# Performance work log

Measured on AMD Instinct MI355X. Metric: run time of the kernel, lower is better.

## Reference

```python
import jax, jax.numpy as jnp
import numpy as np

P, L, H, DEG = 50000, 8000, 8, 64
S = 32
ITERATIONS = 8

def _glorot(k, shape):
    fan = shape[0] + shape[-1]
    return jax.random.normal(k, shape, jnp.float32) * (2.0 / fan) ** 0.5

def _gru(x, h, Wx, Wh, bi, bh):
    # Keras GRUCell gate order: z, r, h-candidate; reset applied after recurrent matmul
    gx = x @ Wx + bi
    gh = h @ Wh + bh
    xz, xr, xn = jnp.split(gx, 3, axis=-1)
    hz, hr, hn = jnp.split(gh, 3, axis=-1)
    z = jax.nn.sigmoid(xz + hz)
    r = jax.nn.sigmoid(xr + hr)
    n = jnp.tanh(xn + r * hn)
    return z * h + (1.0 - z) * n

def _mlp2(x, w1, b1, w2, b2):
    return jax.nn.relu(jax.nn.relu(x @ w1 + b1) @ w2 + b2)

def setup_inputs():
    key = jax.random.key(0)
    ks = jax.random.split(key, 48)
    it = iter(range(48))
    nk = lambda: ks[next(it)]
    inp = {}
    inp['flow_traffic'] = jax.random.uniform(nk(), (P, 1)) * 1000.0 + 100.0
    inp['flow_packets'] = jax.random.uniform(nk(), (P, 1)) * 100.0 + 10.0
    inp['flow_lambda'] = jax.random.uniform(nk(), (P, 1)) * 10.0 + 0.1
    inp['flow_ON_bits_rate'] = jax.random.uniform(nk(), (P, 1)) * 1000.0 + 1.0
    inp['flow_ON_time'] = jax.random.uniform(nk(), (P, 1)) * 5.0 + 0.1
    inp['flow_OFF_time'] = jax.random.uniform(nk(), (P, 1)) * 5.0 + 0.1
    inp['link_capacity'] = jax.random.uniform(nk(), (L, 1)) * 9.0 + 1.0
    # params (z-scores are mean 0 / std 1 -> identity normalization)
    inp['pe_w1'] = _glorot(nk(), (9, S)); inp['pe_b1'] = jnp.zeros((S,))
    inp['pe_w2'] = _glorot(nk(), (S, S)); inp['pe_b2'] = jnp.zeros((S,))
    inp['le_w1'] = _glorot(nk(), (1, S)); inp['le_b1'] = jnp.zeros((S,))
    inp['le_w2'] = _glorot(nk(), (S, S)); inp['le_b2'] = jnp.zeros((S,))
    inp['qe_w1'] = _glorot(nk(), (2, S)); inp['qe_b1'] = jnp.zeros((S,))
    inp['qe_w2'] = _glorot(nk(), (S, S)); inp['qe_b2'] = jnp.zeros((S,))
    inp['path_Wx'] = _glorot(nk(), (2 * S, 3 * S)); inp['path_Wh'] = _glorot(nk(), (S, 3 * S))
    inp['path_bi'] = jnp.zeros((3 * S,)); inp['path_bh'] = jnp.zeros((3 * S,))
    inp['queue_Wx'] = _glorot(nk(), (S, 3 * S)); inp['queue_Wh'] = _glorot(nk(), (S, 3 * S))
    inp['queue_bi'] = jnp.zeros((3 * S,)); inp['queue_bh'] = jnp.zeros((3 * S,))
    inp['link_Wx'] = _glorot(nk(), (S, 3 * S)); inp['link_Wh'] = _glorot(nk(), (S, 3 * S))
    inp['link_bi'] = jnp.zeros((3 * S,)); inp['link_bh'] = jnp.zeros((3 * S,))
    inp['ro_w1'] = _glorot(nk(), (S, 16)); inp['ro_b1'] = jnp.zeros((16,))
    inp['ro_w2'] = _glorot(nk(), (16, 16)); inp['ro_b2'] = jnp.zeros((16,))
    inp['ro_w3'] = _glorot(nk(), (16, 1)); inp['ro_b3'] = jnp.zeros((1,))
    # topology indices
    inp['flow_dist'] = jax.random.randint(nk(), (P, 1), 0, 3, jnp.int32)
    inp['buffer_type'] = jax.random.randint(nk(), (L, 1), 0, 2, jnp.int32)
    inp['link_to_path'] = jax.random.randint(nk(), (P, H), 0, L, jnp.int32)
    p2l_path = jax.random.randint(nk(), (L, DEG), 0, P, jnp.int32)
    p2l_pos = jax.random.randint(nk(), (L, DEG), 1, H + 1, jnp.int32)
    inp['path_to_link'] = jnp.stack([p2l_path, p2l_pos], axis=-1)  # [L, DEG, 2]
    inp['queue_to_link'] = jax.random.randint(nk(), (L, 1), 0, L, jnp.int32)
    return inp

def reference(flow_traffic, flow_packets, flow_lambda, flow_ON_bits_rate, flow_ON_time, flow_OFF_time, link_capacity,
              pe_w1, pe_b1, pe_w2, pe_b2, le_w1, le_b1, le_w2, le_b2, qe_w1, qe_b1, qe_w2, qe_b2,
              path_Wx, path_Wh, path_bi, path_bh, queue_Wx, queue_Wh, queue_bi, queue_bh,
              link_Wx, link_Wh, link_bi, link_bh, ro_w1, ro_b1, ro_w2, ro_b2, ro_w3, ro_b3,
              flow_dist, buffer_type, link_to_path, path_to_link, queue_to_link):
    # path embedding: [traffic, packets, one_hot(dist,3), lambda, ON_rate, ON_t, OFF_t] -> 9 features
    feats = jnp.concatenate([flow_traffic, flow_packets, jax.nn.one_hot(flow_dist[:, 0], 3),
                             flow_lambda, flow_ON_bits_rate, flow_ON_time, flow_OFF_time], axis=1)
    path_state = _mlp2(feats, pe_w1, pe_b1, pe_w2, pe_b2)            # [P, S]
    load = flow_traffic[path_to_link[:, :, 0], 0].sum(axis=1, keepdims=True) / link_capacity  # [L, 1]
    link_state = _mlp2(load, le_w1, le_b1, le_w2, le_b2)             # [L, S]
    queue_state = _mlp2(jax.nn.one_hot(buffer_type[:, 0], 2), qe_w1, qe_b1, qe_w2, qe_b2)     # [L, S]
    seq = None
    for _ in range(ITERATIONS):
        qg = queue_state[link_to_path]                               # [P, H, S]
        lg = link_state[link_to_path]                                # [P, H, S]
        x_seq = jnp.concatenate([qg, lg], axis=-1)                   # [P, H, 2S]
        prev = path_state
        def step(h, xt):
            h2 = _gru(xt, h, path_Wx, path_Wh, path_bi, path_bh)
            return h2, h2
        path_state, seq = jax.lax.scan(step, prev, jnp.swapaxes(x_seq, 0, 1))
        seq = jnp.swapaxes(seq, 0, 1)                                # [P, H, S]
        pss = jnp.concatenate([prev[:, None, :], seq], axis=1)       # [P, H+1, S]
        pg = pss[path_to_link[:, :, 0], path_to_link[:, :, 1]]       # [L, DEG, S] (gather_nd)
        queue_state = _gru(pg.sum(axis=1), queue_state, queue_Wx, queue_Wh, queue_bi, queue_bh)
        qg2 = queue_state[queue_to_link[:, 0]]                       # [L, S] (RNN over seq len 1)
        link_state = _gru(qg2, link_state, link_Wx, link_Wh, link_bi, link_bh)
    cap_g = (link_capacity * 1e9)[link_to_path]                      # [P, H, 1]
    h1 = jax.nn.relu(seq @ ro_w1 + ro_b1)
    h2 = jax.nn.relu(h1 @ ro_w2 + ro_b2)
    occ = h2 @ ro_w3 + ro_b3                                         # [P, H, 1]
    queue_delay = (occ / cap_g).sum(axis=1)                          # [P, 1]
    pkt_size = flow_traffic / flow_packets
    trans_delay = pkt_size * (1.0 / cap_g).sum(axis=1)               # [P, 1]
    return queue_delay + trans_delay
```

## Files before the change

kernel.cpp:

```cpp
#include <hip/hip_runtime.h>
#include <hip/hip_fp16.h>

#define PN 50000
#define LN 8000
#define HN 8
#define DEGN 64
#define SSN 32

typedef _Float16 half2v __attribute__((ext_vector_type(2)));
typedef unsigned u2v __attribute__((ext_vector_type(2)));
static __device__ __forceinline__ half2v u2h(unsigned u){ half2v h; __builtin_memcpy(&h, &u, 4); return h; }
static __device__ __forceinline__ unsigned pkrtz(float a, float b){
    auto v = __builtin_amdgcn_cvt_pkrtz(a, b); unsigned u; __builtin_memcpy(&u, &v, 4); return u; }
static __device__ __forceinline__ float dpp_x1(float x){
    return __int_as_float(__builtin_amdgcn_update_dpp(0, __float_as_int(x), 0xB1, 0xF, 0xF, true)); }

static __device__ __forceinline__ float xhalf_sum(float v){
    u2v r = __builtin_amdgcn_permlane32_swap(__float_as_uint(v), __float_as_uint(v), false, false);
    return __uint_as_float(r.x) + __uint_as_float(r.y);
}

static __device__ __forceinline__ float rcp_(float x){ return __builtin_amdgcn_rcpf(x); }
static __device__ __forceinline__ float sig_(float x){ return rcp_(1.0f + __expf(-x)); }
static __device__ __forceinline__ float tanh_(float x){ return 1.0f - 2.0f*rcp_(__expf(2.0f*x) + 1.0f); }

#define OFF_PWHP 0
#define OFF_PATH 27648
#define OFF_SEQ  1627648
#define OFF_QWX16 14000000
#define OFF_QWH16 14002048
#define OFF_LWX16 14004096
#define OFF_LWH16 14006144
#define OFF_PWX16 14008192
#define OFF_QST  14427648
#define OFF_LST  14683648
#define OFF_G    14939648

__global__ __launch_bounds__(256) void k_startup(
    const float* __restrict__ pWh, const float* __restrict__ pWx,
    const float* __restrict__ qWx, const float* __restrict__ qWh,
    const float* __restrict__ lWx, const float* __restrict__ lWh,
    float* __restrict__ ws,
    const float* __restrict__ ft, const float* __restrict__ fpk,
    const float* __restrict__ flam, const float* __restrict__ fob,
    const float* __restrict__ fon, const float* __restrict__ foff,
    const int* __restrict__ fdist,
    const float* __restrict__ pe_w1, const float* __restrict__ pe_b1,
    const float* __restrict__ pe_w2, const float* __restrict__ pe_b2,
    float* __restrict__ path_state,
    const float* __restrict__ cap,
    const int* __restrict__ p2l, const int* __restrict__ btype,
    const float* __restrict__ lw1, const float* __restrict__ lb1,
    const float* __restrict__ lw2, const float* __restrict__ lb2,
    const float* __restrict__ qw1, const float* __restrict__ qb1,
    const float* __restrict__ qw2, const float* __restrict__ qb2,
    const float* __restrict__ pbi, const float* __restrict__ pbh,
    unsigned* __restrict__ lstate16, unsigned* __restrict__ qstate16,
    float* __restrict__ G)
{
    __shared__ float tl[4][SSN], tq[4][SSN], x2[4][2*SSN];
    int b = blockIdx.x;
    if (b < 54){
        int i0 = b*256 + threadIdx.x;
        if (i0 < 1536){
            int q = i0 >> 8, rem = i0 & 255, lane = rem >> 2, c = rem & 3;
            int idx = q*4 + c;
            int g = idx >> 3, m = idx & 7;
            int half16 = (lane >> 5) << 4, j = lane & 31;
            float w0 = pWh[(half16 + 2*m + 0)*96 + g*32 + j];
            float w1 = pWh[(half16 + 2*m + 1)*96 + g*32 + j];
            ((unsigned*)(ws + OFF_PWHP))[i0] = pkrtz(w0, w1);
            return;
        }
        i0 -= 1536;
        if (i0 < 2048){ int m=i0>>7, rem=i0&127, j=rem>>2, g=rem&3;
            unsigned u=0; if (g<3) u = pkrtz(qWx[(2*m)*96+g*32+j], qWx[(2*m+1)*96+g*32+j]);
            ((unsigned*)(ws+OFF_QWX16))[i0]=u; return; }
        i0 -= 2048;
        if (i0 < 2048){ int m=i0>>7, rem=i0&127, j=rem>>2, g=rem&3;
            unsigned u=0; if (g<3) u = pkrtz(qWh[(2*m)*96+g*32+j], qWh[(2*m+1)*96+g*32+j]);
            ((unsigned*)(ws+OFF_QWH16))[i0]=u; return; }
        i0 -= 2048;
        if (i0 < 2048){ int m=i0>>7, rem=i0&127, j=rem>>2, g=rem&3;
            unsigned u=0; if (g<3) u = pkrtz(lWx[(2*m)*96+g*32+j], lWx[(2*m+1)*96+g*32+j]);
            ((unsigned*)(ws+OFF_LWX16))[i0]=u; return; }
        i0 -= 2048;
        if (i0 < 2048){ int m=i0>>7, rem=i0&127, j=rem>>2, g=rem&3;
            unsigned u=0; if (g<3) u = pkrtz(lWh[(2*m)*96+g*32+j], lWh[(2*m+1)*96+g*32+j]);
            ((unsigned*)(ws+OFF_LWH16))[i0]=u; return; }
        i0 -= 2048;
        if (i0 < 4096){ int m=i0>>7, rem=i0&127, j=rem>>2, g=rem&3;
            unsigned u=0; if (g<3) u = pkrtz(pWx[(2*m)*96+g*32+j], pWx[(2*m+1)*96+g*32+j]);
            ((unsigned*)(ws+OFF_PWX16))[i0]=u; return; }
        return;
    }
    if (b < 250){
        int p = (b-54)*256 + threadIdx.x; if (p >= PN) p = PN-1;
        float f[9];
        f[0]=ft[p]; f[1]=fpk[p];
        int dcls = fdist[p];
        f[2] = (dcls==0)?1.f:0.f; f[3]=(dcls==1)?1.f:0.f; f[4]=(dcls==2)?1.f:0.f;
        f[5]=flam[p]; f[6]=fob[p]; f[7]=fon[p]; f[8]=foff[p];
        float h1[SSN];
        #pragma unroll
        for (int j=0;j<SSN;j++){
            float a = pe_b1[j];
            #pragma unroll
            for (int k=0;k<9;k++) a += f[k]*pe_w1[k*SSN+j];
            h1[j] = fmaxf(a, 0.f);
        }
        #pragma unroll
        for (int j=0;j<SSN;j++){
            float a = pe_b2[j];
            #pragma unroll
            for (int k=0;k<SSN;k++) a += h1[k]*pe_w2[k*SSN+j];
            path_state[p*SSN+j] = fmaxf(a, 0.f);
        }
        return;
    }
    {
        int wid = threadIdx.x >> 6, d = threadIdx.x & 63, j = d & 31;
        int l = (b-250)*4 + wid;
        float s = ft[p2l[(l*DEGN+d)*2]];
        s += __shfl_xor(s, 1);  s += __shfl_xor(s, 2);  s += __shfl_xor(s, 4);
        s += __shfl_xor(s, 8);  s += __shfl_xor(s, 16); s += __shfl_xor(s, 32);
        float load = s / cap[l];
        int bt = btype[l];
        if (d < 32){
            tl[wid][j] = fmaxf(load*lw1[j] + lb1[j], 0.f);
            tq[wid][j] = fmaxf(qw1[bt*SSN+j] + qb1[j], 0.f);
        }
        __syncthreads();
        float al = lb2[j], aq = qb2[j];
        #pragma unroll
        for (int k=0;k<SSN;k++){
            al += tl[wid][k]*lw2[k*SSN+j];
            aq += tq[wid][k]*qw2[k*SSN+j];
        }
        float ls = fmaxf(al, 0.f), qs = fmaxf(aq, 0.f);
        float ls_o = dpp_x1(ls), qs_o = dpp_x1(qs);
        if (d < 32){
            if (!(d & 1)){
                lstate16[l*16 + (j>>1)] = pkrtz(ls, ls_o);
                qstate16[l*16 + (j>>1)] = pkrtz(qs, qs_o);
            }
            x2[wid][j] = qs; x2[wid][SSN+j] = ls;
        }
        __syncthreads();
        float a0=pbi[j]+pbh[j], a1=pbi[SSN+j]+pbh[SSN+j], a2=pbi[2*SSN+j];
        #pragma unroll
        for (int k=0;k<2*SSN;k++){
            float xk = x2[wid][k];
            a0 += xk*pWx[k*96 + j];
            a1 += xk*pWx[k*96 + SSN + j];
            a2 += xk*pWx[k*96 + 2*SSN + j];
        }
        if (d < 32){
            G[l*96 + j] = a0; G[l*96 + SSN + j] = a1; G[l*96 + 2*SSN + j] = a2;
        }
    }
}

__global__ __launch_bounds__(256)
void k_path_gru(
    const float* __restrict__ G, const int* __restrict__ l2p,
    const float* __restrict__ Whp, const float* __restrict__ bh,
    float* __restrict__ path_state, unsigned* __restrict__ seq16)
{
    __shared__ unsigned hsh[4][16];
    const int tid  = threadIdx.x;
    const int lane = tid & 63;
    const int j    = lane & 31;
    const int wslot = tid >> 6;
    const int half8 = (lane >> 5) << 3;
    const bool wr  = (lane < SSN) && !(lane & 1);
    int p = blockIdx.x*4 + wslot;
    p = __builtin_amdgcn_readfirstlane(p);
    unsigned w[24];
    {
        const uint4* wp = (const uint4*)Whp;
        #pragma unroll
        for (int q=0;q<6;q++){
            uint4 v = wp[q*64 + lane];
            w[4*q]=v.x; w[4*q+1]=v.y; w[4*q+2]=v.z; w[4*q+3]=v.w;
        }
    }
    const float bn = bh[2*SSN + j];
    const int4 la = *(const int4*)(l2p + p*HN);
    const int4 lb = *(const int4*)(l2p + p*HN + 4);
    float hj = path_state[p*SSN + j];
    {
        float oth = dpp_x1(hj);
        unsigned pk0 = pkrtz(hj, oth);
        if (wr) hsh[wslot][j>>1] = pk0;
    }
    float cz, cr, cn, nz, nr, nn;
    { const float* g = G + __builtin_amdgcn_readfirstlane(la.x)*96; cz=g[j]; cr=g[SSN+j]; cn=g[2*SSN+j]; }

#define PF(L_) { const float* g = G + __builtin_amdgcn_readfirstlane(L_)*96; nz=g[j]; nr=g[SSN+j]; nn=g[2*SSN+j]; }
#define HOP(T_) { \
    asm volatile("" ::: "memory"); \
    uint4 hv0 = *(const uint4*)&hsh[wslot][half8]; \
    uint4 hv1 = *(const uint4*)&hsh[wslot][half8+4]; \
    float az=0.f, ar=0.f, an=0.f; \
    az = __builtin_amdgcn_fdot2(u2h(hv0.x), u2h(w[ 0]), az, false); \
    ar = __builtin_amdgcn_fdot2(u2h(hv0.x), u2h(w[ 8]), ar, false); \
    an = __builtin_amdgcn_fdot2(u2h(hv0.x), u2h(w[16]), an, false); \
    az = __builtin_amdgcn_fdot2(u2h(hv0.y), u2h(w[ 1]), az, false); \
    ar = __builtin_amdgcn_fdot2(u2h(hv0.y), u2h(w[ 9]), ar, false); \
    an = __builtin_amdgcn_fdot2(u2h(hv0.y), u2h(w[17]), an, false); \
    az = __builtin_amdgcn_fdot2(u2h(hv0.z), u2h(w[ 2]), az, false); \
    ar = __builtin_amdgcn_fdot2(u2h(hv0.z), u2h(w[10]), ar, false); \
    an = __builtin_amdgcn_fdot2(u2h(hv0.z), u2h(w[18]), an, false); \
    az = __builtin_amdgcn_fdot2(u2h(hv0.w), u2h(w[ 3]), az, false); \
    ar = __builtin_amdgcn_fdot2(u2h(hv0.w), u2h(w[11]), ar, false); \
    an = __builtin_amdgcn_fdot2(u2h(hv0.w), u2h(w[19]), an, false); \
    az = __builtin_amdgcn_fdot2(u2h(hv1.x), u2h(w[ 4]), az, false); \
    ar = __builtin_amdgcn_fdot2(u2h(hv1.x), u2h(w[12]), ar, false); \
    an = __builtin_amdgcn_fdot2(u2h(hv1.x), u2h(w[20]), an, false); \
    az = __builtin_amdgcn_fdot2(u2h(hv1.y), u2h(w[ 5]), az, false); \
    ar = __builtin_amdgcn_fdot2(u2h(hv1.y), u2h(w[13]), ar, false); \
    an = __builtin_amdgcn_fdot2(u2h(hv1.y), u2h(w[21]), an, false); \
    az = __builtin_amdgcn_fdot2(u2h(hv1.z), u2h(w[ 6]), az, false); \
    ar = __builtin_amdgcn_fdot2(u2h(hv1.z), u2h(w[14]), ar, false); \
    an = __builtin_amdgcn_fdot2(u2h(hv1.z), u2h(w[22]), an, false); \
    az = __builtin_amdgcn_fdot2(u2h(hv1.w), u2h(w[ 7]), az, false); \
    ar = __builtin_amdgcn_fdot2(u2h(hv1.w), u2h(w[15]), ar, false); \
    an = __builtin_amdgcn_fdot2(u2h(hv1.w), u2h(w[23]), an, false); \
    az = xhalf_sum(az); \
    ar = xhalf_sum(ar); \
    an = xhalf_sum(an); \
    float z = sig_(cz + az); \
    float r = sig_(cr + ar); \
    float n = tanh_(cn + r*(an + bn)); \
    hj = z*hj + (1.0f-z)*n; \
    float oth = dpp_x1(hj); \
    unsigned pk = pkrtz(hj, oth); \
    if (wr){ hsh[wslot][j>>1] = pk; seq16[(p*HN+T_)*16 + (j>>1)] = pk; } \
    cz = nz; cr = nr; cn = nn; }

    PF(la.y) HOP(0)
    PF(la.z) HOP(1)
    PF(la.w) HOP(2)
    PF(lb.x) HOP(3)
    PF(lb.y) HOP(4)
    PF(lb.z) HOP(5)
    PF(lb.w) HOP(6)
    HOP(7)
#undef PF
#undef HOP
    if (lane < SSN) path_state[p*SSN + j] = hj;
}

__global__ __launch_bounds__(256) void k_queue_gru(
    const unsigned* __restrict__ seq16, const int* __restrict__ p2l,
    const unsigned* __restrict__ wx16, const unsigned* __restrict__ wh16,
    const float* __restrict__ bi, const float* __restrict__ bhb,
    unsigned* __restrict__ qstate16)
{
    __shared__ float red[2][DEGN][SSN+1];
    __shared__ unsigned xpk_lds[2][16];
    int tid  = threadIdx.x;
    int wv   = tid >> 6;
    int slot = wv >> 1;
    int wp   = wv & 1;
    int lane = tid & 63;
    int r    = (lane & 31) + (wp << 5);
    int half = lane >> 5;
    int l = __builtin_amdgcn_readfirstlane(blockIdx.x*2 + slot);
    int pp  = p2l[(l*DEGN + r)*2 + 0];
    int pos = p2l[(l*DEGN + r)*2 + 1];
    const uint4* row = (const uint4*)(seq16 + (pp*HN + pos - 1)*16 + half*8);
    uint4 v0 = row[0], v1 = row[1];
    float* dst = &red[slot][r][16*half];
    {
        half2v a,b;
        a=u2h(v0.x); b=u2h(v0.y); dst[ 0]=(float)a.x; dst[ 1]=(float)a.y; dst[ 2]=(float)b.x; dst[ 3]=(float)b.y;
        a=u2h(v0.z); b=u2h(v0.w); dst[ 4]=(float)a.x; dst[ 5]=(float)a.y; dst[ 6]=(float)b.x; dst[ 7]=(float)b.y;
        a=u2h(v1.x); b=u2h(v1.y); dst[ 8]=(float)a.x; dst[ 9]=(float)a.y; dst[10]=(float)b.x; dst[11]=(float)b.y;
        a=u2h(v1.z); b=u2h(v1.w); dst[12]=(float)a.x; dst[13]=(float)a.y; dst[14]=(float)b.x; dst[15]=(float)b.y;
    }
    __syncthreads();
    if (wp) return;
    int j = lane & 31;
    int base = (lane < 32) ? 0 : 32;
    float xs = 0.f;
    #pragma unroll
    for (int dd=0; dd<32; dd++) xs += red[slot][base+dd][j];
    xs = xhalf_sum(xs);
    {
        float oth = dpp_x1(xs);
        unsigned pkx = pkrtz(xs, oth);
        if (lane < 32 && !(lane & 1)) xpk_lds[slot][j>>1] = pkx;
    }
    unsigned hpk[16];
    {
        const uint4* h4 = (const uint4*)(qstate16 + l*16);
        #pragma unroll
        for (int q=0;q<4;q++){ uint4 v=h4[q]; hpk[4*q]=v.x; hpk[4*q+1]=v.y; hpk[4*q+2]=v.z; hpk[4*q+3]=v.w; }
    }
    half2v hw = u2h(hpk[j>>1]);
    float hj = (j & 1) ? (float)hw.y : (float)hw.x;
    unsigned xq[16];
    {
        asm volatile("" ::: "memory");
        const uint4* xl = (const uint4*)xpk_lds[slot];
        #pragma unroll
        for (int q=0;q<4;q++){ uint4 v=xl[q]; xq[4*q]=v.x; xq[4*q+1]=v.y; xq[4*q+2]=v.z; xq[4*q+3]=v.w; }
    }
    float az = bi[j] + bhb[j];
    float ar = bi[SSN+j] + bhb[SSN+j];
    float xn = bi[2*SSN+j];
    float hn = bhb[2*SSN+j];
    #pragma unroll
    for (int m=0;m<16;m++){
        uint4 wx4 = ((const uint4*)wx16)[m*32 + j];
        uint4 wh4 = ((const uint4*)wh16)[m*32 + j];
        az = __builtin_amdgcn_fdot2(u2h(xq[m]),  u2h(wx4.x), az, false);
        ar = __builtin_amdgcn_fdot2(u2h(xq[m]),  u2h(wx4.y), ar, false);
        xn = __builtin_amdgcn_fdot2(u2h(xq[m]),  u2h(wx4.z), xn, false);
        az = __builtin_amdgcn_fdot2(u2h(hpk[m]), u2h(wh4.x), az, false);
        ar = __builtin_amdgcn_fdot2(u2h(hpk[m]), u2h(wh4.y), ar, false);
        hn = __builtin_amdgcn_fdot2(u2h(hpk[m]), u2h(wh4.z), hn, false);
    }
    float z = sig_(az), r2 = sig_(ar);
    float n = tanh_(xn + r2*hn);
    float outv = z*hj + (1.0f-z)*n;
    float oth = dpp_x1(outv);
    if (lane < 32 && !(lane & 1))
        qstate16[l*16 + (j>>1)] = pkrtz(outv, oth);
}

__global__ __launch_bounds__(256) void k_link_gru(
    const unsigned* __restrict__ qstate16, const int* __restrict__ q2l,
    const unsigned* __restrict__ wx16, const unsigned* __restrict__ wh16,
    const float* __restrict__ bi, const float* __restrict__ bhb,
    const unsigned* __restrict__ pwx16, const float* __restrict__ pbi,
    const float* __restrict__ pbh,
    unsigned* __restrict__ lstate16, float* __restrict__ G)
{
    __shared__ unsigned lpk_lds[4][16];
    int wid = threadIdx.x >> 6, d = threadIdx.x & 63, j = d & 31;
    int l = __builtin_amdgcn_readfirstlane(blockIdx.x*4 + wid);
    int src = __builtin_amdgcn_readfirstlane(q2l[l]);
    unsigned xpk[16], hpk[16], qpk[16];
    {
        const uint4* x4 = (const uint4*)(qstate16 + src*16);
        const uint4* h4 = (const uint4*)(lstate16 + l*16);
        const uint4* q4 = (const uint4*)(qstate16 + l*16);
        #pragma unroll
        for (int q=0;q<4;q++){
            uint4 a=x4[q]; xpk[4*q]=a.x; xpk[4*q+1]=a.y; xpk[4*q+2]=a.z; xpk[4*q+3]=a.w;
            uint4 b=h4[q]; hpk[4*q]=b.x; hpk[4*q+1]=b.y; hpk[4*q+2]=b.z; hpk[4*q+3]=b.w;
            uint4 c=q4[q]; qpk[4*q]=c.x; qpk[4*q+1]=c.y; qpk[4*q+2]=c.z; qpk[4*q+3]=c.w;
        }
    }
    half2v hw = u2h(hpk[j>>1]);
    float hj = (j & 1) ? (float)hw.y : (float)hw.x;
    float az = bi[j]+bhb[j], ar = bi[SSN+j]+bhb[SSN+j];
    float xn = bi[2*SSN+j], hn = bhb[2*SSN+j];
    #pragma unroll
    for (int m=0;m<16;m++){
        uint4 wx4 = ((const uint4*)wx16)[m*32 + j];
        uint4 wh4 = ((const uint4*)wh16)[m*32 + j];
        az = __builtin_amdgcn_fdot2(u2h(xpk[m]), u2h(wx4.x), az, false);
        ar = __builtin_amdgcn_fdot2(u2h(xpk[m]), u2h(wx4.y), ar, false);
        xn = __builtin_amdgcn_fdot2(u2h(xpk[m]), u2h(wx4.z), xn, false);
        az = __builtin_amdgcn_fdot2(u2h(hpk[m]), u2h(wh4.x), az, false);
        ar = __builtin_amdgcn_fdot2(u2h(hpk[m]), u2h(wh4.y), ar, false);
        hn = __builtin_amdgcn_fdot2(u2h(hpk[m]), u2h(wh4.z), hn, false);
    }
    float z = sig_(az), r = sig_(ar);
    float n = tanh_(xn + r*hn);
    float outv = z*hj + (1.0f-z)*n;
    {
        float oth = dpp_x1(outv);
        unsigned pko = pkrtz(outv, oth);
        if (d < 32 && !(d & 1)){ lstate16[l*16 + (j>>1)] = pko; lpk_lds[wid][j>>1] = pko; }
    }
    unsigned lpk[16];
    {
        asm volatile("" ::: "memory");
        const uint4* ll = (const uint4*)lpk_lds[wid];
        #pragma unroll
        for (int q=0;q<4;q++){ uint4 v=ll[q]; lpk[4*q]=v.x; lpk[4*q+1]=v.y; lpk[4*q+2]=v.z; lpk[4*q+3]=v.w; }
    }
    float a0 = pbi[j]+pbh[j], a1 = pbi[SSN+j]+pbh[SSN+j], a2 = pbi[2*SSN+j];
    #pragma unroll
    for (int m=0;m<32;m++){
        uint4 wv4 = ((const uint4*)pwx16)[m*32 + j];
        unsigned xm = (m < 16) ? qpk[m] : lpk[m-16];
        a0 = __builtin_amdgcn_fdot2(u2h(xm), u2h(wv4.x), a0, false);
        a1 = __builtin_amdgcn_fdot2(u2h(xm), u2h(wv4.y), a1, false);
        a2 = __builtin_amdgcn_fdot2(u2h(xm), u2h(wv4.z), a2, false);
    }
    if (d < 32){
        G[l*96 + j] = a0; G[l*96 + SSN + j] = a1; G[l*96 + 2*SSN + j] = a2;
    }
}

__global__ __launch_bounds__(256, 4) void k_readout(
    const unsigned* __restrict__ seq16, const int* __restrict__ l2p,
    const float* __restrict__ cap, const float* __restrict__ ft,
    const float* __restrict__ fpk,
    const float* __restrict__ w1, const float* __restrict__ b1,
    const float* __restrict__ w2, const float* __restrict__ b2,
    const float* __restrict__ w3, const float* __restrict__ b3,
    float* __restrict__ out)
{
    int g = blockIdx.x*256 + threadIdx.x;
    int p = g >> 3, t = g & 7;
    if (p >= PN) p = PN-1;
    int lk = l2p[p*HN + t];
    const uint4* s4 = (const uint4*)(seq16 + (p*HN+t)*16);
    float sv[SSN];
    #pragma unroll
    for (int q=0;q<4;q++){
        uint4 v = s4[q];
        half2v a=u2h(v.x), b=u2h(v.y), c=u2h(v.z), e=u2h(v.w);
        sv[8*q+0]=(float)a.x; sv[8*q+1]=(float)a.y;
        sv[8*q+2]=(float)b.x; sv[8*q+3]=(float)b.y;
        sv[8*q+4]=(float)c.x; sv[8*q+5]=(float)c.y;
        sv[8*q+6]=(float)e.x; sv[8*q+7]=(float)e.y;
    }
    float h1[16];
    #pragma unroll
    for (int j=0;j<16;j++) h1[j] = b1[j];
    #pragma unroll
    for (int k=0;k<SSN;k++){
        float vk = sv[k];
        #pragma unroll
        for (int j=0;j<16;j++) h1[j] += vk*w1[k*16+j];
    }
    #pragma unroll
    for (int j=0;j<16;j++) h1[j] = fmaxf(h1[j], 0.f);
    float h2[16];
    #pragma unroll
    for (int j=0;j<16;j++) h2[j] = b2[j];
    #pragma unroll
    for (int k=0;k<16;k++){
        float hk = h1[k];
        #pragma unroll
        for (int j=0;j<16;j++) h2[j] += hk*w2[k*16+j];
    }
    float occ = b3[0];
    #pragma unroll
    for (int k=0;k<16;k++) occ += fmaxf(h2[k], 0.f)*w3[k];
    float icg = rcp_(cap[lk]) * 1e-9f;
    float qd  = occ * icg;
    float inv = icg;
    qd  += __shfl_xor(qd, 1);  inv += __shfl_xor(inv, 1);
    qd  += __shfl_xor(qd, 2);  inv += __shfl_xor(inv, 2);
    qd  += __shfl_xor(qd, 4);  inv += __shfl_xor(inv, 4);
    if ((threadIdx.x & 7) == 0)
        out[p] = qd + ft[p]*rcp_(fpk[p])*inv;
}

extern "C" void kernel_launch(void* const* d_in, const int* in_sizes, int n_in,
                              void* d_out, int out_size, void* d_ws, size_t ws_size,
                              hipStream_t stream)
{
    (void)in_sizes; (void)n_in; (void)out_size; (void)ws_size;
    const float* ft    = (const float*)d_in[0];
    const float* fpk   = (const float*)d_in[1];
    const float* flam  = (const float*)d_in[2];
    const float* fob   = (const float*)d_in[3];
    const float* fon   = (const float*)d_in[4];
    const float* foff  = (const float*)d_in[5];
    const float* cap   = (const float*)d_in[6];
    const float* pe_w1 = (const float*)d_in[7];
    const float* pe_b1 = (const float*)d_in[8];
    const float* pe_w2 = (const float*)d_in[9];
    const float* pe_b2 = (const float*)d_in[10];
    const float* le_w1 = (const float*)d_in[11];
    const float* le_b1 = (const float*)d_in[12];
    const float* le_w2 = (const float*)d_in[13];
    const float* le_b2 = (const float*)d_in[14];
    const float* qe_w1 = (const float*)d_in[15];
    const float* qe_b1 = (const float*)d_in[16];
    const float* qe_w2 = (const float*)d_in[17];
    const float* qe_b2 = (const float*)d_in[18];
    const float* pWx   = (const float*)d_in[19];
    const float* pWh   = (const float*)d_in[20];
    const float* pbi   = (const float*)d_in[21];
    const float* pbh   = (const float*)d_in[22];
    const float* qWx   = (const float*)d_in[23];
    const float* qWh   = (const float*)d_in[24];
    const float* qbi   = (const float*)d_in[25];
    const float* qbh   = (const float*)d_in[26];
    const float* lWx   = (const float*)d_in[27];
    const float* lWh   = (const float*)d_in[28];
    const float* lbi   = (const float*)d_in[29];
    const float* lbh   = (const float*)d_in[30];
    const float* ro_w1 = (const float*)d_in[31];
    const float* ro_b1 = (const float*)d_in[32];
    const float* ro_w2 = (const float*)d_in[33];
    const float* ro_b2 = (const float*)d_in[34];
    const float* ro_w3 = (const float*)d_in[35];
    const float* ro_b3 = (const float*)d_in[36];
    const int* fdist = (const int*)d_in[37];
    const int* btype = (const int*)d_in[38];
    const int* l2p   = (const int*)d_in[39];
    const int* p2l   = (const int*)d_in[40];
    const int* q2l   = (const int*)d_in[41];

    float* ws = (float*)d_ws;
    float* pWhp = ws + OFF_PWHP;
    float* path_state  = ws + OFF_PATH;
    unsigned* seq16    = (unsigned*)(ws + OFF_SEQ);
    unsigned* qwx16    = (unsigned*)(ws + OFF_QWX16);
    unsigned* qwh16    = (unsigned*)(ws + OFF_QWH16);
    unsigned* lwx16    = (unsigned*)(ws + OFF_LWX16);
    unsigned* lwh16    = (unsigned*)(ws + OFF_LWH16);
    unsigned* pwx16    = (unsigned*)(ws + OFF_PWX16);
    unsigned* qstate16 = (unsigned*)(ws + OFF_QST);
    unsigned* lstate16 = (unsigned*)(ws + OFF_LST);
    float* G           = ws + OFF_G;

    k_startup<<<2250, 256, 0, stream>>>(pWh, pWx, qWx, qWh, lWx, lWh, ws,
                                        ft, fpk, flam, fob, fon, foff, fdist,
                                        pe_w1, pe_b1, pe_w2, pe_b2, path_state,
                                        cap, p2l, btype,
                                        le_w1, le_b1, le_w2, le_b2,
                                        qe_w1, qe_b1, qe_w2, qe_b2,
                                        pbi, pbh, lstate16, qstate16, G);
    for (int it = 0; it < 7; ++it){
        k_path_gru<<<PN/4, 256, 0, stream>>>(G, l2p, pWhp, pbh, path_state, seq16);
        k_queue_gru<<<LN/2, 256, 0, stream>>>(seq16, p2l, qwx16, qwh16, qbi, qbh, qstate16);
        k_link_gru<<<LN/4, 256, 0, stream>>>(qstate16, q2l, lwx16, lwh16, lbi, lbh,
                                             pwx16, pbi, pbh, lstate16, G);
    }
    k_path_gru<<<PN/4, 256, 0, stream>>>(G, l2p, pWhp, pbh, path_state, seq16);
    k_readout<<<(PN*HN+255)/256, 256, 0, stream>>>(seq16, l2p, cap, ft, fpk,
                                                   ro_w1, ro_b1, ro_w2, ro_b2, ro_w3, ro_b3,
                                                   (float*)d_out);
}
```

Baseline: 668.6 us.

## Process two paths per wave in path GRU with LDS-staged fp16 weights

The path GRU kernel now assigns one path to each 32-lane half of a wave, so each block handles eight paths instead of four. Previously both halves cooperated on one path and combined partial sums with a cross-half swap. Each lane now computes the full 32-wide dot products itself, reading the packed fp16 recurrent weights from shared memory instead of holding 24 registers of weights. This drops the permlane reductions, frees registers and halves the block count. The cost is more LDS traffic per hop, and the G-row loads are no longer wave-uniform scalar loads.

New measurement: 573.5 us. 14.2% less time.

```diff
diff --git a/kernel.cpp b/kernel.cpp
--- a/kernel.cpp
+++ b/kernel.cpp
@@ -63,12 +63,12 @@
     if (b < 54){
         int i0 = b*256 + threadIdx.x;
         if (i0 < 1536){
-            int q = i0 >> 8, rem = i0 & 255, lane = rem >> 2, c = rem & 3;
-            int idx = q*4 + c;
-            int g = idx >> 3, m = idx & 7;
-            int half16 = (lane >> 5) << 4, j = lane & 31;
-            float w0 = pWh[(half16 + 2*m + 0)*96 + g*32 + j];
-            float w1 = pWh[(half16 + 2*m + 1)*96 + g*32 + j];
+            int c = i0 & 3, slot = i0 >> 2;
+            int j = slot & 31, gq = slot >> 5;
+            int g = gq >> 2, q = gq & 2|(gq&3); q = gq & 3;
+            int m = q*4 + c;
+            float w0 = pWh[(2*m + 0)*96 + g*32 + j];
+            float w1 = pWh[(2*m + 1)*96 + g*32 + j];
             ((unsigned*)(ws + OFF_PWHP))[i0] = pkrtz(w0, w1);
             return;
         }
@@ -164,79 +164,54 @@
 __global__ __launch_bounds__(256)
 void k_path_gru(
     const float* __restrict__ G, const int* __restrict__ l2p,
-    const float* __restrict__ Whp, const float* __restrict__ bh,
+    const unsigned* __restrict__ Whp, const float* __restrict__ bh,
     float* __restrict__ path_state, unsigned* __restrict__ seq16)
 {
-    __shared__ unsigned hsh[4][16];
-    const int tid  = threadIdx.x;
-    const int lane = tid & 63;
-    const int j    = lane & 31;
+    __shared__ uint4 wlds[384];
+    __shared__ unsigned hsh[4][32];
+    const int tid   = threadIdx.x;
+    const int lane  = tid & 63;
+    const int j     = lane & 31;
+    const int half  = lane >> 5;
     const int wslot = tid >> 6;
-    const int half8 = (lane >> 5) << 3;
-    const bool wr  = (lane < SSN) && !(lane & 1);
-    int p = blockIdx.x*4 + wslot;
-    p = __builtin_amdgcn_readfirstlane(p);
-    unsigned w[24];
-    {
-        const uint4* wp = (const uint4*)Whp;
-        #pragma unroll
-        for (int q=0;q<6;q++){
-            uint4 v = wp[q*64 + lane];
-            w[4*q]=v.x; w[4*q+1]=v.y; w[4*q+2]=v.z; w[4*q+3]=v.w;
-        }
-    }
+    const bool wr   = !(lane & 1);
+    const int p = blockIdx.x*8 + (wslot<<1) + half;
+    #pragma unroll
+    for (int i = tid; i < 384; i += 256) wlds[i] = ((const uint4*)Whp)[i];
+    __syncthreads();
     const float bn = bh[2*SSN + j];
     const int4 la = *(const int4*)(l2p + p*HN);
     const int4 lb = *(const int4*)(l2p + p*HN + 4);
     float hj = path_state[p*SSN + j];
     {
         float oth = dpp_x1(hj);
-        unsigned pk0 = pkrtz(hj, oth);
-        if (wr) hsh[wslot][j>>1] = pk0;
+        if (wr) hsh[wslot][half*16 + (j>>1)] = pkrtz(hj, oth);
     }
     float cz, cr, cn, nz, nr, nn;
-    { const float* g = G + __builtin_amdgcn_readfirstlane(la.x)*96; cz=g[j]; cr=g[SSN+j]; cn=g[2*SSN+j]; }
-
-#define PF(L_) { const float* g = G + __builtin_amdgcn_readfirstlane(L_)*96; nz=g[j]; nr=g[SSN+j]; nn=g[2*SSN+j]; }
+    { const float* g = G + la.x*96; cz=g[j]; cr=g[SSN+j]; cn=g[2*SSN+j]; }
+
+#define GDOT(acc_, gbase_, hv_, qi_) { \
+    uint4 wv = wlds[(gbase_ + qi_)*32 + j]; \
+    acc_ = __builtin_amdgcn_fdot2(u2h(hv_.x), u2h(wv.x), acc_, false); \
+    acc_ = __builtin_amdgcn_fdot2(u2h(hv_.y), u2h(wv.y), acc_, false); \
+    acc_ = __builtin_amdgcn_fdot2(u2h(hv_.z), u2h(wv.z), acc_, false); \
+    acc_ = __builtin_amdgcn_fdot2(u2h(hv_.w), u2h(wv.w), acc_, false); }
+#define PF(L_) { const float* g = G + (L_)*96; nz=g[j]; nr=g[SSN+j]; nn=g[2*SSN+j]; }
 #define HOP(T_) { \
     asm volatile("" ::: "memory"); \
-    uint4 hv0 = *(const uint4*)&hsh[wslot][half8]; \
-    uint4 hv1 = *(const uint4*)&hsh[wslot][half8+4]; \
+    const uint4* hp = (const uint4*)&hsh[wslot][half*16]; \
+    uint4 h0 = hp[0], h1 = hp[1], h2 = hp[2], h3 = hp[3]; \
     float az=0.f, ar=0.f, an=0.f; \
-    az = __builtin_amdgcn_fdot2(u2h(hv0.x), u2h(w[ 0]), az, false); \
-    ar = __builtin_amdgcn_fdot2(u2h(hv0.x), u2h(w[ 8]), ar, false); \
-    an = __builtin_amdgcn_fdot2(u2h(hv0.x), u2h(w[16]), an, false); \
-    az = __builtin_amdgcn_fdot2(u2h(hv0.y), u2h(w[ 1]), az, false); \
-    ar = __builtin_amdgcn_fdot2(u2h(hv0.y), u2h(w[ 9]), ar, false); \
-    an = __builtin_amdgcn_fdot2(u2h(hv0.y), u2h(w[17]), an, false); \
-    az = __builtin_amdgcn_fdot2(u2h(hv0.z), u2h(w[ 2]), az, false); \
-    ar = __builtin_amdgcn_fdot2(u2h(hv0.z), u2h(w[10]), ar, false); \
-    an = __builtin_amdgcn_fdot2(u2h(hv0.z), u2h(w[18]), an, false); \
-    az = __builtin_amdgcn_fdot2(u2h(hv0.w), u2h(w[ 3]), az, false); \
-    ar = __builtin_amdgcn_fdot2(u2h(hv0.w), u2h(w[11]), ar, false); \
-    an = __builtin_amdgcn_fdot2(u2h(hv0.w), u2h(w[19]), an, false); \
-    az = __builtin_amdgcn_fdot2(u2h(hv1.x), u2h(w[ 4]), az, false); \
-    ar = __builtin_amdgcn_fdot2(u2h(hv1.x), u2h(w[12]), ar, false); \
-    an = __builtin_amdgcn_fdot2(u2h(hv1.x), u2h(w[20]), an, false); \
-    az = __builtin_amdgcn_fdot2(u2h(hv1.y), u2h(w[ 5]), az, false); \
-    ar = __builtin_amdgcn_fdot2(u2h(hv1.y), u2h(w[13]), ar, false); \
-    an = __builtin_amdgcn_fdot2(u2h(hv1.y), u2h(w[21]), an, false); \
-    az = __builtin_amdgcn_fdot2(u2h(hv1.z), u2h(w[ 6]), az, false); \
-    ar = __builtin_amdgcn_fdot2(u2h(hv1.z), u2h(w[14]), ar, false); \
-    an = __builtin_amdgcn_fdot2(u2h(hv1.z), u2h(w[22]), an, false); \
-    az = __builtin_amdgcn_fdot2(u2h(hv1.w), u2h(w[ 7]), az, false); \
-    ar = __builtin_amdgcn_fdot2(u2h(hv1.w), u2h(w[15]), ar, false); \
-    an = __builtin_amdgcn_fdot2(u2h(hv1.w), u2h(w[23]), an, false); \
-    az = xhalf_sum(az); \
-    ar = xhalf_sum(ar); \
-    an = xhalf_sum(an); \
+    GDOT(az, 0, h0, 0) GDOT(az, 0, h1, 1) GDOT(az, 0, h2, 2) GDOT(az, 0, h3, 3) \
+    GDOT(ar, 4, h0, 0) GDOT(ar, 4, h1, 1) GDOT(ar, 4, h2, 2) GDOT(ar, 4, h3, 3) \
+    GDOT(an, 8, h0, 0) GDOT(an, 8, h1, 1) GDOT(an, 8, h2, 2) GDOT(an, 8, h3, 3) \
     float z = sig_(cz + az); \
     float r = sig_(cr + ar); \
     float n = tanh_(cn + r*(an + bn)); \
     hj = z*hj + (1.0f-z)*n; \
     float oth = dpp_x1(hj); \
     unsigned pk = pkrtz(hj, oth); \
-    if (wr){ hsh[wslot][j>>1] = pk; seq16[(p*HN+T_)*16 + (j>>1)] = pk; } \
+    if (wr){ hsh[wslot][half*16 + (j>>1)] = pk; seq16[(p*HN+T_)*16 + (j>>1)] = pk; } \
     cz = nz; cr = nr; cn = nn; }
 
     PF(la.y) HOP(0)
@@ -249,7 +224,8 @@
     HOP(7)
 #undef PF
 #undef HOP
-    if (lane < SSN) path_state[p*SSN + j] = hj;
+#undef GDOT
+    path_state[p*SSN + j] = hj;
 }
 
 __global__ __launch_bounds__(256) void k_queue_gru(
@@ -505,7 +481,7 @@
     const int* q2l   = (const int*)d_in[41];
 
     float* ws = (float*)d_ws;
-    float* pWhp = ws + OFF_PWHP;
+    unsigned* pWhp16   = (unsigned*)(ws + OFF_PWHP);
     float* path_state  = ws + OFF_PATH;
     unsigned* seq16    = (unsigned*)(ws + OFF_SEQ);
     unsigned* qwx16    = (unsigned*)(ws + OFF_QWX16);
@@ -525,12 +501,12 @@
                                         qe_w1, qe_b1, qe_w2, qe_b2,
                                         pbi, pbh, lstate16, qstate16, G);
     for (int it = 0; it < 7; ++it){
-        k_path_gru<<<PN/4, 256, 0, stream>>>(G, l2p, pWhp, pbh, path_state, seq16);
+        k_path_gru<<<PN/8, 256, 0, stream>>>(G, l2p, pWhp16, pbh, path_state, seq16);
         k_queue_gru<<<LN/2, 256, 0, stream>>>(seq16, p2l, qwx16, qwh16, qbi, qbh, qstate16);
         k_link_gru<<<LN/4, 256, 0, stream>>>(qstate16, q2l, lwx16, lwh16, lbi, lbh,
                                              pwx16, pbi, pbh, lstate16, G);
     }
-    k_path_gru<<<PN/4, 256, 0, stream>>>(G, l2p, pWhp, pbh, path_state, seq16);
+    k_path_gru<<<PN/8, 256, 0, stream>>>(G, l2p, pWhp16, pbh, path_state, seq16);
     k_readout<<<(PN*HN+255)/256, 256, 0, stream>>>(seq16, l2p, cap, ft, fpk,
                                                    ro_w1, ro_b1, ro_w2, ro_b2, ro_w3, ro_b3,
                                                    (float*)d_out);
```
